# Kernel optimization log

Hardware: AMD Instinct MI355X
Metric: run time of the kernel (lower is better)

The kernel has to match this reference:

```python
import jax, jax.numpy as jnp
import numpy as np

N_EMBD = 1024
N_HEAD = 16
HEAD_DIM = N_EMBD // N_HEAD
EPS = 1e-5


def setup_inputs() -> dict:
    key = jax.random.key(0)
    ks = jax.random.split(key, 6)
    B, S, D = 2, 2048, N_EMBD
    s = 0.02
    return {
        "x": jax.random.normal(ks[0], (B, S, D), jnp.float32),
        "ln1_g": jnp.ones((D,), jnp.float32),
        "ln1_b": jnp.zeros((D,), jnp.float32),
        "w_attn": jax.random.normal(ks[1], (D, 3 * D), jnp.float32) * s,
        "b_attn": jnp.zeros((3 * D,), jnp.float32),
        "w_attn_proj": jax.random.normal(ks[2], (D, D), jnp.float32) * s,
        "b_attn_proj": jnp.zeros((D,), jnp.float32),
        "ln2_g": jnp.ones((D,), jnp.float32),
        "ln2_b": jnp.zeros((D,), jnp.float32),
        "w_fc": jax.random.normal(ks[3], (D, 4 * D), jnp.float32) * s,
        "b_fc": jnp.zeros((4 * D,), jnp.float32),
        "w_fc_proj": jax.random.normal(ks[4], (4 * D, D), jnp.float32) * s,
        "b_fc_proj": jnp.zeros((D,), jnp.float32),
    }


def _layernorm(x, g, b):
    mu = jnp.mean(x, axis=-1, keepdims=True)
    var = jnp.mean(jnp.square(x - mu), axis=-1, keepdims=True)
    return (x - mu) * jax.lax.rsqrt(var + EPS) * g + b


def _block(x, ln1_g, ln1_b, w_attn, b_attn, w_attn_proj, b_attn_proj,
           ln2_g, ln2_b, w_fc, b_fc, w_fc_proj, b_fc_proj):
    B, S, D = x.shape
    h = _layernorm(x, ln1_g, ln1_b)
    qkv = h @ w_attn + b_attn                       # [B,S,3D]
    q, k, v = jnp.split(qkv, 3, axis=-1)
    # [B,H,S,hd]
    q = q.reshape(B, S, N_HEAD, HEAD_DIM).transpose(0, 2, 1, 3)
    k = k.reshape(B, S, N_HEAD, HEAD_DIM).transpose(0, 2, 1, 3)
    v = v.reshape(B, S, N_HEAD, HEAD_DIM).transpose(0, 2, 1, 3)
    scores = jnp.einsum("bhqd,bhkd->bhqk", q, k) / jnp.sqrt(
        jnp.asarray(HEAD_DIM, x.dtype))
    causal = jnp.tril(jnp.ones((S, S), bool))
    scores = jnp.where(causal, scores, -jnp.inf)
    attn = jax.nn.softmax(scores, axis=-1)
    out = jnp.einsum("bhqk,bhkd->bhqd", attn, v)    # [B,H,S,hd]
    out = out.transpose(0, 2, 1, 3).reshape(B, S, D)
    x = x + (out @ w_attn_proj + b_attn_proj)
    h2 = _layernorm(x, ln2_g, ln2_b)
    m = jax.nn.gelu(h2 @ w_fc + b_fc, approximate=False)
    x = x + (m @ w_fc_proj + b_fc_proj)
    return x


def reference(x, ln1_g, ln1_b, w_attn, b_attn, w_attn_proj, b_attn_proj,
              ln2_g, ln2_b, w_fc, b_fc, w_fc_proj, b_fc_proj):
    return _block(x, ln1_g, ln1_b, w_attn, b_attn, w_attn_proj, b_attn_proj,
                  ln2_g, ln2_b, w_fc, b_fc, w_fc_proj, b_fc_proj)
```

## Files before the change

### kernel.cpp

```cpp
#include <hip/hip_runtime.h>
#include <hip/hip_bf16.h>
#include <math.h>

typedef __bf16 bf16_t;
typedef bf16_t bf16x8 __attribute__((ext_vector_type(8)));
typedef float f32x4 __attribute__((ext_vector_type(4)));
typedef unsigned short u16;
typedef u16 ushort8 __attribute__((ext_vector_type(8)));

static __device__ __forceinline__ u16 f2bf(float f) {
    unsigned u = __builtin_bit_cast(unsigned, f);
    u += 0x7FFFu + ((u >> 16) & 1u);
    return (u16)(u >> 16);
}

__global__ __launch_bounds__(256) void ln_kernel(
    const float* __restrict__ x, const float* __restrict__ g,
    const float* __restrict__ be, u16* __restrict__ out)
{
    const int row = blockIdx.x;
    const int tid = threadIdx.x;
    const float4 v = ((const float4*)(x + (long)row * 1024))[tid];
    float s = v.x + v.y + v.z + v.w;
#pragma unroll
    for (int d = 32; d >= 1; d >>= 1) s += __shfl_xor(s, d);
    __shared__ float r1[4], r2[4];
    if ((tid & 63) == 0) r1[tid >> 6] = s;
    __syncthreads();
    const float mean = (r1[0] + r1[1] + r1[2] + r1[3]) * (1.0f / 1024.0f);
    const float dx = v.x - mean, dy = v.y - mean, dz = v.z - mean, dw = v.w - mean;
    float sq = dx * dx + dy * dy + dz * dz + dw * dw;
#pragma unroll
    for (int d = 32; d >= 1; d >>= 1) sq += __shfl_xor(sq, d);
    if ((tid & 63) == 0) r2[tid >> 6] = sq;
    __syncthreads();
    const float var = (r2[0] + r2[1] + r2[2] + r2[3]) * (1.0f / 1024.0f);
    const float rstd = rsqrtf(var + 1e-5f);
    const float4 gg = ((const float4*)g)[tid];
    const float4 bb = ((const float4*)be)[tid];
    ushort4 o;
    o.x = f2bf(dx * rstd * gg.x + bb.x);
    o.y = f2bf(dy * rstd * gg.y + bb.y);
    o.z = f2bf(dz * rstd * gg.z + bb.z);
    o.w = f2bf(dw * rstd * gg.w + bb.w);
    *(ushort4*)&out[(long)row * 1024 + tid * 4] = o;
}

__global__ __launch_bounds__(256) void tcvt_kernel(
    const float* __restrict__ in, u16* __restrict__ outT, int R, int C)
{
    __shared__ float tile[32][33];
    const int tx = threadIdx.x, ty = threadIdx.y;
    const int c0 = blockIdx.x * 32, r0 = blockIdx.y * 32;
#pragma unroll
    for (int i = 0; i < 4; ++i)
        tile[ty + i * 8][tx] = in[(long)(r0 + ty + i * 8) * C + c0 + tx];
    __syncthreads();
#pragma unroll
    for (int i = 0; i < 4; ++i)
        outT[(long)(c0 + ty + i * 8) * R + r0 + tx] = f2bf(tile[tx][ty + i * 8]);
}

template <int BM, int EPI>
__global__ __launch_bounds__(256) void gemm_bt(
    const u16* __restrict__ A, const u16* __restrict__ Bt,
    const float* __restrict__ bias, const float* __restrict__ resid,
    void* __restrict__ C, int M, int N, int K)
{
    constexpr int WN = (BM == 128) ? 2 : 4;
    constexpr int MR = BM / (4 / WN) / 16;
    constexpr int NR = 128 / WN / 16;
    __shared__ __align__(16) u16 As[BM * 32];
    __shared__ __align__(16) u16 Bs[128 * 32];
    const int tid = threadIdx.x;
    const int lane = tid & 63;
    const int w = tid >> 6;
    const int wm = w / WN, wn = w % WN;
    const int bm = blockIdx.x, bn = blockIdx.y;
    f32x4 acc[MR][NR] = {};

    const u16* Ablk = A + (long)bm * BM * K;
    const u16* Bblk = Bt + (long)bn * 128 * K;

    for (int kb = 0; kb < K; kb += 32) {
        __syncthreads();
#pragma unroll
        for (int i = 0; i < BM / 64; ++i) {
            const int o = (w * (BM / 64) + i) * 512 + lane * 8;
            const int row = o >> 5, kk = o & 31;
            __builtin_amdgcn_global_load_lds(
                (const __attribute__((address_space(1))) void*)(Ablk + (long)row * K + kb + kk),
                (__attribute__((address_space(3))) void*)(As + (w * (BM / 64) + i) * 512),
                16, 0, 0);
        }
#pragma unroll
        for (int i = 0; i < 2; ++i) {
            const int o = (w * 2 + i) * 512 + lane * 8;
            const int row = o >> 5, kk = o & 31;
            __builtin_amdgcn_global_load_lds(
                (const __attribute__((address_space(1))) void*)(Bblk + (long)row * K + kb + kk),
                (__attribute__((address_space(3))) void*)(Bs + (w * 2 + i) * 512),
                16, 0, 0);
        }
        __syncthreads();
        bf16x8 af[MR], bfr[NR];
#pragma unroll
        for (int m = 0; m < MR; ++m)
            af[m] = *(const bf16x8*)&As[(wm * MR * 16 + m * 16 + (lane & 15)) * 32 + (lane >> 4) * 8];
#pragma unroll
        for (int n = 0; n < NR; ++n)
            bfr[n] = *(const bf16x8*)&Bs[(wn * NR * 16 + n * 16 + (lane & 15)) * 32 + (lane >> 4) * 8];
#pragma unroll
        for (int m = 0; m < MR; ++m)
#pragma unroll
            for (int n = 0; n < NR; ++n)
                acc[m][n] = __builtin_amdgcn_mfma_f32_16x16x32_bf16(af[m], bfr[n], acc[m][n], 0, 0, 0);
    }

    const int rowBase = bm * BM + wm * MR * 16;
    const int colBase = bn * 128 + wn * NR * 16;
#pragma unroll
    for (int n = 0; n < NR; ++n) {
        const int col = colBase + n * 16 + (lane & 15);
        const float bv = bias[col];
#pragma unroll
        for (int m = 0; m < MR; ++m) {
#pragma unroll
            for (int r = 0; r < 4; ++r) {
                const int row = rowBase + m * 16 + (lane >> 4) * 4 + r;
                float v = acc[m][n][r] + bv;
                if constexpr (EPI == 1) v = 0.5f * v * (1.0f + erff(v * 0.70710678118654752f));
                if constexpr (EPI == 2) {
                    ((float*)C)[(long)row * N + col] = v + resid[(long)row * N + col];
                } else {
                    ((u16*)C)[(long)row * N + col] = f2bf(v);
                }
            }
        }
    }
}

__global__ __launch_bounds__(256) void attn_kernel(
    const u16* __restrict__ qkv, u16* __restrict__ outb)
{
    const int S = 2048;
    const int ipair = blockIdx.x;
    const int bh = blockIdx.y;
    const int b = bh >> 4, h = bh & 15;
    const int tid = threadIdx.x, lane = tid & 63, w = tid >> 6;
    __shared__ __align__(16) u16 Ks[2][64 * 72];
    __shared__ __align__(16) u16 Vs[2][64 * 72];
    __shared__ __align__(16) u16 Ps[4][16 * 72];

    const long base = (long)b * S * 3072;
    const int rstage = tid >> 3;
    const int cg = (tid & 7) * 8;
    const int sw = cg;
    const u16* kbase = qkv + base + 1024 + h * 64 + cg;
    const u16* vbase = qkv + base + 2048 + h * 64 + cg;

    for (int half = 0; half < 2; ++half) {
        const int qt = half ? 31 - ipair : ipair;
        const int q0 = qt * 64;

        bf16x8 qf[2];
        {
            const int qrow = q0 + w * 16 + (lane & 15);
#pragma unroll
            for (int c = 0; c < 2; ++c)
                qf[c] = *(const bf16x8*)&qkv[base + (long)qrow * 3072 + h * 64 + c * 32 + (lane >> 4) * 8];
        }

        f32x4 Of[4] = {};
        float mrow[4], lrow[4];
#pragma unroll
        for (int r = 0; r < 4; ++r) { mrow[r] = -1e30f; lrow[r] = 0.0f; }

        ushort8 kr[2], vr[2];
#pragma unroll
        for (int it = 0; it < 2; ++it) {
            const long ro = (long)(it * 32 + rstage) * 3072;
            kr[it] = *(const ushort8*)&kbase[ro];
            vr[it] = *(const ushort8*)&vbase[ro];
        }
        __syncthreads();
#pragma unroll
        for (int it = 0; it < 2; ++it) {
            const int r = it * 32 + rstage;
            *(ushort8*)&Ks[0][r * 72 + cg] = kr[it];
#pragma unroll
            for (int j = 0; j < 8; ++j)
                Vs[0][(cg + j) * 72 + (r ^ sw)] = vr[it][j];
        }

        for (int kt = 0; kt <= qt; ++kt) {
            const int cur = kt & 1;
            if (kt < qt) {
#pragma unroll
                for (int it = 0; it < 2; ++it) {
                    const long ro = (long)((kt + 1) * 64 + it * 32 + rstage) * 3072;
                    kr[it] = *(const ushort8*)&kbase[ro];
                    vr[it] = *(const ushort8*)&vbase[ro];
                }
            }
            __syncthreads();

            f32x4 Sf[4] = {};
#pragma unroll
            for (int f = 0; f < 4; ++f) {
#pragma unroll
                for (int c = 0; c < 2; ++c) {
                    const bf16x8 kf = *(const bf16x8*)&Ks[cur][(f * 16 + (lane & 15)) * 72 + c * 32 + (lane >> 4) * 8];
                    Sf[f] = __builtin_amdgcn_mfma_f32_16x16x32_bf16(qf[c], kf, Sf[f], 0, 0, 0);
                }
            }
#pragma unroll
            for (int f = 0; f < 4; ++f)
#pragma unroll
                for (int r = 0; r < 4; ++r)
                    Sf[f][r] *= 0.125f;
            if (kt == qt) {
#pragma unroll
                for (int f = 0; f < 4; ++f) {
                    const int kvc = f * 16 + (lane & 15);
#pragma unroll
                    for (int r = 0; r < 4; ++r) {
                        const int qr = w * 16 + (lane >> 4) * 4 + r;
                        if (kvc > qr) Sf[f][r] = -1e30f;
                    }
                }
            }
            float mnew[4], sc[4];
#pragma unroll
            for (int r = 0; r < 4; ++r) {
                float mx = fmaxf(fmaxf(Sf[0][r], Sf[1][r]), fmaxf(Sf[2][r], Sf[3][r]));
#pragma unroll
                for (int d = 1; d < 16; d <<= 1) mx = fmaxf(mx, __shfl_xor(mx, d));
                mnew[r] = fmaxf(mrow[r], mx);
                sc[r] = __expf(mrow[r] - mnew[r]);
                mrow[r] = mnew[r];
            }
#pragma unroll
            for (int f = 0; f < 4; ++f)
#pragma unroll
                for (int r = 0; r < 4; ++r)
                    Sf[f][r] = __expf(Sf[f][r] - mnew[r]);
#pragma unroll
            for (int r = 0; r < 4; ++r) {
                float s = Sf[0][r] + Sf[1][r] + Sf[2][r] + Sf[3][r];
#pragma unroll
                for (int d = 1; d < 16; d <<= 1) s += __shfl_xor(s, d);
                lrow[r] = lrow[r] * sc[r] + s;
            }
#pragma unroll
            for (int f = 0; f < 4; ++f)
#pragma unroll
                for (int r = 0; r < 4; ++r)
                    Of[f][r] *= sc[r];
#pragma unroll
            for (int f = 0; f < 4; ++f)
#pragma unroll
                for (int r = 0; r < 4; ++r)
                    Ps[w][((lane >> 4) * 4 + r) * 72 + f * 16 + (lane & 15)] = f2bf(Sf[f][r]);
#pragma unroll
            for (int f = 0; f < 4; ++f) {
                const int hd = f * 16 + (lane & 15);
#pragma unroll
                for (int c = 0; c < 2; ++c) {
                    const int k0 = c * 32 + (lane >> 4) * 8;
                    const bf16x8 pa = *(const bf16x8*)&Ps[w][(lane & 15) * 72 + k0];
                    const bf16x8 vb = *(const bf16x8*)&Vs[cur][hd * 72 + (k0 ^ (hd & 56))];
                    Of[f] = __builtin_amdgcn_mfma_f32_16x16x32_bf16(pa, vb, Of[f], 0, 0, 0);
                }
            }
            if (kt < qt) {
#pragma unroll
                for (int it = 0; it < 2; ++it) {
                    const int r = it * 32 + rstage;
                    *(ushort8*)&Ks[cur ^ 1][r * 72 + cg] = kr[it];
#pragma unroll
                    for (int j = 0; j < 8; ++j)
                        Vs[cur ^ 1][(cg + j) * 72 + (r ^ sw)] = vr[it][j];
                }
            }
        }

        float inv[4];
#pragma unroll
        for (int r = 0; r < 4; ++r) inv[r] = 1.0f / lrow[r];
#pragma unroll
        for (int f = 0; f < 4; ++f) {
            const int col = h * 64 + f * 16 + (lane & 15);
#pragma unroll
            for (int r = 0; r < 4; ++r) {
                const int qrow = q0 + w * 16 + (lane >> 4) * 4 + r;
                outb[((long)b * S + qrow) * 1024 + col] = f2bf(Of[f][r] * inv[r]);
            }
        }
    }
}

extern "C" void kernel_launch(void* const* d_in, const int* in_sizes, int n_in,
                              void* d_out, int out_size, void* d_ws, size_t ws_size,
                              hipStream_t stream) {
    const float* x      = (const float*)d_in[0];
    const float* ln1_g  = (const float*)d_in[1];
    const float* ln1_b  = (const float*)d_in[2];
    const float* w_attn = (const float*)d_in[3];
    const float* b_attn = (const float*)d_in[4];
    const float* w_ap   = (const float*)d_in[5];
    const float* b_ap   = (const float*)d_in[6];
    const float* ln2_g  = (const float*)d_in[7];
    const float* ln2_b  = (const float*)d_in[8];
    const float* w_fc   = (const float*)d_in[9];
    const float* b_fc   = (const float*)d_in[10];
    const float* w_fp   = (const float*)d_in[11];
    const float* b_fp   = (const float*)d_in[12];
    float* out = (float*)d_out;

    const int R = 4096;
    char* p = (char*)d_ws;
    u16*   wTa  = (u16*)(p);
    u16*   wTap = (u16*)(p + 6291456);
    u16*   wTfc = (u16*)(p + 8388608);
    u16*   wTfp = (u16*)(p + 16777216);
    u16*   hao  = (u16*)(p + 25165824);
    u16*   qkv  = (u16*)(p + 33554432);
    u16*   mb   = hao;
    u16*   h2   = wTa;
    float* x1   = out;

    const dim3 tb(32, 8);
    tcvt_kernel<<<dim3(3072 / 32, 1024 / 32), tb, 0, stream>>>(w_attn, wTa, 1024, 3072);
    tcvt_kernel<<<dim3(1024 / 32, 1024 / 32), tb, 0, stream>>>(w_ap, wTap, 1024, 1024);
    tcvt_kernel<<<dim3(4096 / 32, 1024 / 32), tb, 0, stream>>>(w_fc, wTfc, 1024, 4096);
    tcvt_kernel<<<dim3(1024 / 32, 4096 / 32), tb, 0, stream>>>(w_fp, wTfp, 4096, 1024);

    ln_kernel<<<R, 256, 0, stream>>>(x, ln1_g, ln1_b, hao);
    gemm_bt<128, 0><<<dim3(32, 24), 256, 0, stream>>>(hao, wTa, b_attn, nullptr, qkv, R, 3072, 1024);
    attn_kernel<<<dim3(16, 32), 256, 0, stream>>>(qkv, hao);
    gemm_bt<64, 2><<<dim3(64, 8), 256, 0, stream>>>(hao, wTap, b_ap, x, x1, R, 1024, 1024);
    ln_kernel<<<R, 256, 0, stream>>>(x1, ln2_g, ln2_b, h2);
    gemm_bt<128, 1><<<dim3(32, 32), 256, 0, stream>>>(h2, wTfc, b_fc, nullptr, mb, R, 4096, 1024);
    gemm_bt<64, 2><<<dim3(64, 8), 256, 0, stream>>>(mb, wTfp, b_fp, x1, out, R, 1024, 4096);
}
```

Measured before the change: 312.9 us.

## Double-buffer GEMM LDS tiles with async prefetch and use tanh GELU

The GEMM body now keeps two LDS buffers for A and B and prefetches the next K tile with global_load_lds while computing on the current one, using explicit vmcnt waits and barriers instead of syncthreads on both sides. The goal is to hide global-load latency behind MFMA work. The FC epilogue also swaps exact erf GELU for the tanh approximation written through a sigmoid with __expf, which trades accuracy for cheaper math. Each template instance is wrapped in its own named kernel; MR is hardcoded to 4, which matches both the BM=128 and BM=64 configurations.

Measured after the change: 292.0 us. -6.7%, faster.

```diff
diff --git a/kernel.cpp b/kernel.cpp
--- a/kernel.cpp
+++ b/kernel.cpp
@@ -62,16 +62,18 @@
 }
 
 template <int BM, int EPI>
-__global__ __launch_bounds__(256) void gemm_bt(
+static __device__ __forceinline__ void gemm_body(
     const u16* __restrict__ A, const u16* __restrict__ Bt,
     const float* __restrict__ bias, const float* __restrict__ resid,
     void* __restrict__ C, int M, int N, int K)
 {
     constexpr int WN = (BM == 128) ? 2 : 4;
-    constexpr int MR = BM / (4 / WN) / 16;
+    constexpr int MR = 4;
     constexpr int NR = 128 / WN / 16;
-    __shared__ __align__(16) u16 As[BM * 32];
-    __shared__ __align__(16) u16 Bs[128 * 32];
+    constexpr int AI = BM / 64;
+    constexpr int LPW = AI + 2;
+    __shared__ __align__(16) u16 As[2][BM * 32];
+    __shared__ __align__(16) u16 Bs[2][128 * 32];
     const int tid = threadIdx.x;
     const int lane = tid & 63;
     const int w = tid >> 6;
@@ -81,16 +83,16 @@
 
     const u16* Ablk = A + (long)bm * BM * K;
     const u16* Bblk = Bt + (long)bn * 128 * K;
-
-    for (int kb = 0; kb < K; kb += 32) {
-        __syncthreads();
-#pragma unroll
-        for (int i = 0; i < BM / 64; ++i) {
-            const int o = (w * (BM / 64) + i) * 512 + lane * 8;
+    const int nt = K >> 5;
+
+    auto stage = [&](int buf, int kb) {
+#pragma unroll
+        for (int i = 0; i < AI; ++i) {
+            const int o = (w * AI + i) * 512 + lane * 8;
             const int row = o >> 5, kk = o & 31;
             __builtin_amdgcn_global_load_lds(
                 (const __attribute__((address_space(1))) void*)(Ablk + (long)row * K + kb + kk),
-                (__attribute__((address_space(3))) void*)(As + (w * (BM / 64) + i) * 512),
+                (__attribute__((address_space(3))) void*)(&As[buf][(w * AI + i) * 512]),
                 16, 0, 0);
         }
 #pragma unroll
@@ -99,22 +101,40 @@
             const int row = o >> 5, kk = o & 31;
             __builtin_amdgcn_global_load_lds(
                 (const __attribute__((address_space(1))) void*)(Bblk + (long)row * K + kb + kk),
-                (__attribute__((address_space(3))) void*)(Bs + (w * 2 + i) * 512),
+                (__attribute__((address_space(3))) void*)(&Bs[buf][(w * 2 + i) * 512]),
                 16, 0, 0);
         }
-        __syncthreads();
+    };
+
+    stage(0, 0);
+    for (int t = 0; t < nt; ++t) {
+        const int cur = t & 1;
+        if (t + 1 < nt) {
+            stage(cur ^ 1, (t + 1) << 5);
+            asm volatile("s_waitcnt vmcnt(%0)" :: "i"(LPW) : "memory");
+        } else {
+            asm volatile("s_waitcnt vmcnt(0)" ::: "memory");
+        }
+        __builtin_amdgcn_s_barrier();
+        asm volatile("" ::: "memory");
+
         bf16x8 af[MR], bfr[NR];
 #pragma unroll
         for (int m = 0; m < MR; ++m)
-            af[m] = *(const bf16x8*)&As[(wm * MR * 16 + m * 16 + (lane & 15)) * 32 + (lane >> 4) * 8];
+            af[m] = *(const bf16x8*)&As[cur][(wm * MR * 16 + m * 16 + (lane & 15)) * 32 + (lane >> 4) * 8];
 #pragma unroll
         for (int n = 0; n < NR; ++n)
-            bfr[n] = *(const bf16x8*)&Bs[(wn * NR * 16 + n * 16 + (lane & 15)) * 32 + (lane >> 4) * 8];
+            bfr[n] = *(const bf16x8*)&Bs[cur][(wn * NR * 16 + n * 16 + (lane & 15)) * 32 + (lane >> 4) * 8];
 #pragma unroll
         for (int m = 0; m < MR; ++m)
 #pragma unroll
             for (int n = 0; n < NR; ++n)
                 acc[m][n] = __builtin_amdgcn_mfma_f32_16x16x32_bf16(af[m], bfr[n], acc[m][n], 0, 0, 0);
+
+        if (t + 1 < nt) {
+            asm volatile("" ::: "memory");
+            __builtin_amdgcn_s_barrier();
+        }
     }
 
     const int rowBase = bm * BM + wm * MR * 16;
@@ -129,7 +149,10 @@
             for (int r = 0; r < 4; ++r) {
                 const int row = rowBase + m * 16 + (lane >> 4) * 4 + r;
                 float v = acc[m][n][r] + bv;
-                if constexpr (EPI == 1) v = 0.5f * v * (1.0f + erff(v * 0.70710678118654752f));
+                if constexpr (EPI == 1) {
+                    const float u = v + 0.044715f * v * v * v;
+                    v = v / (1.0f + __expf(-1.5957691216057308f * u));
+                }
                 if constexpr (EPI == 2) {
                     ((float*)C)[(long)row * N + col] = v + resid[(long)row * N + col];
                 } else {
@@ -139,6 +162,19 @@
         }
     }
 }
+
+__global__ __launch_bounds__(256) void gemm_qkv(
+    const u16* A, const u16* Bt, const float* bias, const float* resid,
+    void* C, int M, int N, int K) { gemm_body<128, 0>(A, Bt, bias, resid, C, M, N, K); }
+__global__ __launch_bounds__(256) void gemm_fc(
+    const u16* A, const u16* Bt, const float* bias, const float* resid,
+    void* C, int M, int N, int K) { gemm_body<128, 1>(A, Bt, bias, resid, C, M, N, K); }
+__global__ __launch_bounds__(256) void gemm_ap(
+    const u16* A, const u16* Bt, const float* bias, const float* resid,
+    void* C, int M, int N, int K) { gemm_body<64, 2>(A, Bt, bias, resid, C, M, N, K); }
+__global__ __launch_bounds__(256) void gemm_fp(
+    const u16* A, const u16* Bt, const float* bias, const float* resid,
+    void* C, int M, int N, int K) { gemm_body<64, 2>(A, Bt, bias, resid, C, M, N, K); }
 
 __global__ __launch_bounds__(256) void attn_kernel(
     const u16* __restrict__ qkv, u16* __restrict__ outb)
@@ -337,10 +373,10 @@
     tcvt_kernel<<<dim3(1024 / 32, 4096 / 32), tb, 0, stream>>>(w_fp, wTfp, 4096, 1024);
 
     ln_kernel<<<R, 256, 0, stream>>>(x, ln1_g, ln1_b, hao);
-    gemm_bt<128, 0><<<dim3(32, 24), 256, 0, stream>>>(hao, wTa, b_attn, nullptr, qkv, R, 3072, 1024);
+    gemm_qkv<<<dim3(32, 24), 256, 0, stream>>>(hao, wTa, b_attn, nullptr, qkv, R, 3072, 1024);
     attn_kernel<<<dim3(16, 32), 256, 0, stream>>>(qkv, hao);
-    gemm_bt<64, 2><<<dim3(64, 8), 256, 0, stream>>>(hao, wTap, b_ap, x, x1, R, 1024, 1024);
+    gemm_ap<<<dim3(64, 8), 256, 0, stream>>>(hao, wTap, b_ap, x, x1, R, 1024, 1024);
     ln_kernel<<<R, 256, 0, stream>>>(x1, ln2_g, ln2_b, h2);
-    gemm_bt<128, 1><<<dim3(32, 32), 256, 0, stream>>>(h2, wTfc, b_fc, nullptr, mb, R, 4096, 1024);
-    gemm_bt<64, 2><<<dim3(64, 8), 256, 0, stream>>>(mb, wTfp, b_fp, x1, out, R, 1024, 4096);
-}
+    gemm_fc<<<dim3(32, 32), 256, 0, stream>>>(h2, wTfc, b_fc, nullptr, mb, R, 4096, 1024);
+    gemm_fp<<<dim3(64, 8), 256, 0, stream>>>(mb, wTfp, b_fp, x1, out, R, 1024, 4096);
+}
```
